# Performance work log

Measured on AMD Instinct MI355X. Metric: run time of the kernel, lower is better.

## Reference

```python
import jax, jax.numpy as jnp
import numpy as np

B, S, H = 2, 2048, 2048
NH, NKV = 16, 4
HD = H // NH          # 128
N_REP = NH // NKV     # 4


def _rotate_half(x):
    x1, x2 = x[..., : x.shape[-1] // 2], x[..., x.shape[-1] // 2 :]
    return jnp.concatenate((-x2, x1), axis=-1)


def setup_inputs() -> dict:
    key = jax.random.key(0)
    ks = jax.random.split(key, 5)
    hidden_states = jax.random.normal(ks[0], (B, S, H), dtype=jnp.float32)
    # true rotary tables [max_seq_len, head_dim]
    inv_freq = 1.0 / (10000.0 ** (np.arange(0, HD, 2, dtype=np.float32) / HD))
    t = np.arange(S, dtype=np.float32)
    freqs = np.outer(t, inv_freq)                    # [S, HD/2]
    emb = np.concatenate([freqs, freqs], axis=-1)    # [S, HD]
    cos = jnp.asarray(np.cos(emb))
    sin = jnp.asarray(np.sin(emb))
    Wq = jax.random.normal(ks[1], (H, NH * HD), dtype=jnp.float32) * 0.02
    Wk = jax.random.normal(ks[2], (H, NKV * HD), dtype=jnp.float32) * 0.02
    Wv = jax.random.normal(ks[3], (H, NKV * HD), dtype=jnp.float32) * 0.02
    Wo = jax.random.normal(ks[4], (NH * HD, H), dtype=jnp.float32) * 0.02
    attention_mask = jnp.ones((B, S), dtype=jnp.float32)  # 1 = keep
    return {"hidden_states": hidden_states, "cos": cos, "sin": sin,
            "Wq": Wq, "Wk": Wk, "Wv": Wv, "Wo": Wo,
            "attention_mask": attention_mask}


def reference(hidden_states, cos, sin, Wq, Wk, Wv, Wo, attention_mask):
    # Decoder self-attention: is_causal=True, use_rope=True, no cache, eval (dropout off).
    x = hidden_states
    b, s, _ = x.shape
    q = jnp.einsum('bsh,hd->bsd', x, Wq).reshape(b, s, NH, HD).transpose(0, 2, 1, 3)   # [b,nh,s,hd]
    k = jnp.einsum('bsh,hd->bsd', x, Wk).reshape(b, s, NKV, HD)
    v = jnp.einsum('bsh,hd->bsd', x, Wv).reshape(b, s, NKV, HD)
    # GQA repeat_kv: each kv head repeated n_rep times contiguously
    k = jnp.repeat(k, N_REP, axis=2).transpose(0, 2, 1, 3)   # [b,nh,s,hd]
    v = jnp.repeat(v, N_REP, axis=2).transpose(0, 2, 1, 3)
    # RoPE
    c = cos[:s][None, None, :, :]
    sn = sin[:s][None, None, :, :]
    q = q * c + _rotate_half(q) * sn
    k = k * c + _rotate_half(k) * sn
    # attention scores
    scores = jnp.einsum('bhqd,bhkd->bhqk', q, k) / jnp.sqrt(jnp.float32(HD))
    neg_inf = jnp.finfo(scores.dtype).min
    causal = jnp.triu(jnp.full((s, s), neg_inf, dtype=scores.dtype), k=1)
    scores = scores + causal[None, None, :, :]
    pad = (1.0 - attention_mask[:, None, None, :].astype(scores.dtype)) * neg_inf
    scores = scores + pad
    attn = jax.nn.softmax(scores.astype(jnp.float32), axis=-1).astype(q.dtype)
    out = jnp.einsum('bhqk,bhkd->bhqd', attn, v)             # [b,nh,s,hd]
    out = out.transpose(0, 2, 1, 3).reshape(b, s, NH * HD)
    return jnp.einsum('bsd,dh->bsh', out, Wo)
```

## Files before the change

### kernel.cpp

```cpp
#include <hip/hip_runtime.h>
#include <hip/hip_bf16.h>


typedef __bf16 bf16;
typedef __bf16 bf16x8 __attribute__((ext_vector_type(8)));
typedef __bf16 bf16x4 __attribute__((ext_vector_type(4)));
typedef float  f32x4  __attribute__((ext_vector_type(4)));

#define MFMA_BF16(a, b, c) __builtin_amdgcn_mfma_f32_16x16x32_bf16((a), (b), (c), 0, 0, 0)

__device__ __forceinline__ void glds16(const bf16* g, char* l) {
  __builtin_amdgcn_global_load_lds((__attribute__((address_space(1))) const void*)g,
                                   (__attribute__((address_space(3))) void*)l, 16, 0, 0);
}

__global__ __launch_bounds__(256) void k_cvt_bf16(const float* __restrict__ in,
                                                  bf16* __restrict__ out, int n4) {
  int i = blockIdx.x * 256 + threadIdx.x;
  if (i < n4) {
    float4 v = ((const float4*)in)[i];
    bf16x4 o;
    o[0] = (bf16)v.x; o[1] = (bf16)v.y; o[2] = (bf16)v.z; o[3] = (bf16)v.w;
    ((bf16x4*)out)[i] = o;
  }
}

__global__ __launch_bounds__(256) void k_transpose_w4(const float* __restrict__ Wq,
                                                      const float* __restrict__ Wk,
                                                      const float* __restrict__ Wv,
                                                      const float* __restrict__ Wo,
                                                      bf16* __restrict__ Wtq,
                                                      bf16* __restrict__ Wtk,
                                                      bf16* __restrict__ Wtv,
                                                      bf16* __restrict__ Wto) {
  int z = blockIdx.z;
  const float* W; bf16* Wt; int N;
  if (z == 0)      { W = Wq; Wt = Wtq; N = 2048; }
  else if (z == 1) { W = Wo; Wt = Wto; N = 2048; }
  else if (z == 2) { W = Wk; Wt = Wtk; N = 512; }
  else             { W = Wv; Wt = Wtv; N = 512; }
  int nb = blockIdx.y * 32;
  if (nb >= N) return;
  __shared__ float tile[32][33];
  int tx = threadIdx.x, ty = threadIdx.y;
  int kb = blockIdx.x * 32;
#pragma unroll
  for (int i = 0; i < 4; ++i)
    tile[ty + i * 8][tx] = W[(size_t)(kb + ty + i * 8) * N + nb + tx];
  __syncthreads();
#pragma unroll
  for (int i = 0; i < 4; ++i)
    Wt[(size_t)(nb + ty + i * 8) * 2048 + kb + tx] = (bf16)tile[tx][ty + i * 8];
}

template <typename OUT>
__device__ void gemm_block(const bf16* __restrict__ A, const bf16* __restrict__ Bt,
                           OUT* __restrict__ C, int K, int ldc,
                           int rbase, int cbase, char* sm,
                           float rope_scl, const float* __restrict__ cosb,
                           const float* __restrict__ sinb,
                           bf16* __restrict__ vtr, int vkv) {
  const int tid = threadIdx.x;
  const int lane = tid & 63, wid = tid >> 6;
  const int l15 = lane & 15, lg = lane >> 4;
  char* Asm = sm;
  char* Bsm = sm + 32768;

  f32x4 acc[2][8];
#pragma unroll
  for (int i = 0; i < 2; ++i)
#pragma unroll
    for (int j = 0; j < 8; ++j)
#pragma unroll
      for (int r = 0; r < 4; ++r) acc[i][j][r] = 0.0f;

  const int ob = wid * 4096 + lane * 16;
  auto stage = [&](int buf, int kb) {
#pragma unroll
    for (int c = 0; c < 4; ++c) {
      int o = ob + c * 1024;
      int r = o >> 7;
      int cc = ((o >> 4) & 7) ^ (r & 7);
      int dst = wid * 4096 + c * 1024 + buf * 16384;
      glds16(A + (size_t)(rbase + r) * K + kb + cc * 8, Asm + dst);
      glds16(Bt + (size_t)(cbase + r) * K + kb + cc * 8, Bsm + dst);
    }
  };

  stage(0, 0);
  __syncthreads();
  const int nk = K >> 6;
  for (int t = 0; t < nk; ++t) {
    if (t + 1 < nk) stage((t + 1) & 1, (t + 1) << 6);
    const char* At  = Asm + (t & 1) * 16384;
    const char* Bti = Bsm + (t & 1) * 16384;
#pragma unroll
    for (int ks = 0; ks < 2; ++ks) {
      bf16x8 a[2], b[8];
#pragma unroll
      for (int rf = 0; rf < 2; ++rf) {
        int r = wid * 32 + rf * 16 + l15;
        int slot = (ks * 4 + lg) ^ (r & 7);
        a[rf] = *(const bf16x8*)(At + r * 128 + slot * 16);
      }
#pragma unroll
      for (int nf = 0; nf < 8; ++nf) {
        int n = nf * 16 + l15;
        int slot = (ks * 4 + lg) ^ (n & 7);
        b[nf] = *(const bf16x8*)(Bti + n * 128 + slot * 16);
      }
#pragma unroll
      for (int rf = 0; rf < 2; ++rf)
#pragma unroll
        for (int nf = 0; nf < 8; ++nf)
          acc[rf][nf] = MFMA_BF16(a[rf], b[nf], acc[rf][nf]);
    }
    __syncthreads();
  }

  if (rope_scl != 0.0f) {
#pragma unroll
    for (int rf = 0; rf < 2; ++rf)
#pragma unroll
      for (int r = 0; r < 4; ++r) {
        int s = (rbase + wid * 32 + rf * 16 + lg * 4 + r) & 2047;
#pragma unroll
        for (int nf = 0; nf < 4; ++nf) {
          int d = nf * 16 + l15;
          float v0 = acc[rf][nf][r], v1 = acc[rf][nf + 4][r];
          float c0 = cosb[s * 128 + d],      c1 = cosb[s * 128 + d + 64];
          float s0 = sinb[s * 128 + d],      s1 = sinb[s * 128 + d + 64];
          acc[rf][nf][r]     = (v0 * c0 - v1 * s0) * rope_scl;
          acc[rf][nf + 4][r] = (v1 * c1 + v0 * s1) * rope_scl;
        }
      }
  }

  if (vtr != nullptr) {
#pragma unroll
    for (int rf = 0; rf < 2; ++rf)
#pragma unroll
      for (int nf = 0; nf < 8; ++nf) {
        int s0 = wid * 32 + rf * 16 + lg * 4;
        int d = nf * 16 + l15;
        bf16x4 pk;
#pragma unroll
        for (int r = 0; r < 4; ++r) pk[r] = (bf16)acc[rf][nf][r];
        *(bf16x4*)(sm + d * 256 + ((s0 * 2) ^ ((d & 15) << 4))) = pk;
      }
    __syncthreads();
    const int b4 = (rbase >> 11) * 4;
    const int scol = rbase & 2047;
    const int so = tid & 15;
#pragma unroll
    for (int i = 0; i < 8; ++i) {
      int d = (tid >> 4) + i * 16;
      bf16x8 v = *(const bf16x8*)(sm + d * 256 + ((so * 16) ^ ((d & 15) << 4)));
      *(bf16x8*)(vtr + (size_t)((b4 + vkv) * 128 + d) * 2048 + scol + so * 8) = v;
    }
    return;
  }

#pragma unroll
  for (int rf = 0; rf < 2; ++rf)
#pragma unroll
    for (int nf = 0; nf < 8; ++nf)
#pragma unroll
      for (int r = 0; r < 4; ++r) {
        int row = rbase + wid * 32 + rf * 16 + lg * 4 + r;
        int col = cbase + nf * 16 + l15;
        C[(size_t)row * ldc + col] = (OUT)acc[rf][nf][r];
      }
}

__global__ __launch_bounds__(256, 2) void k_gemm_qkv(const bf16* __restrict__ X,
                                                     const bf16* __restrict__ Wtq,
                                                     const bf16* __restrict__ Wtk,
                                                     const bf16* __restrict__ Wtv,
                                                     bf16* __restrict__ Q,
                                                     bf16* __restrict__ Ko,
                                                     bf16* __restrict__ Vt,
                                                     const float* __restrict__ cosb,
                                                     const float* __restrict__ sinb,
                                                     float sclq) {
  __shared__ alignas(16) char sm[65536];
  int nb = blockIdx.y;
  int rbase = blockIdx.x * 128;
  if (nb < 16) {
    gemm_block<bf16>(X, Wtq, Q, 2048, 2048, rbase, nb * 128, sm, sclq, cosb, sinb,
                     nullptr, 0);
  } else if (nb < 20) {
    gemm_block<bf16>(X, Wtk, Ko, 2048, 512, rbase, (nb - 16) * 128, sm, 1.0f, cosb, sinb,
                     nullptr, 0);
  } else {
    gemm_block<bf16>(X, Wtv, (bf16*)nullptr, 2048, 512, rbase, (nb - 20) * 128, sm,
                     0.0f, nullptr, nullptr, Vt, nb - 20);
  }
}

__global__ __launch_bounds__(256, 2) void k_gemm_o(const bf16* __restrict__ AO,
                                                   const bf16* __restrict__ Wto,
                                                   float* __restrict__ Out) {
  __shared__ alignas(16) char sm[65536];
  gemm_block<float>(AO, Wto, Out, 2048, 2048, blockIdx.x * 128, blockIdx.y * 128, sm,
                    0.0f, nullptr, nullptr, nullptr, 0);
}

__global__ __launch_bounds__(256, 4) void k_fattn(const bf16* __restrict__ Qg,
                                                  const bf16* __restrict__ Kg,
                                                  const bf16* __restrict__ Vtg,
                                                  bf16* __restrict__ AO) {
  __shared__ alignas(16) char sm[37888];
  const int lane = threadIdx.x & 63, wid = threadIdx.x >> 6;
  const int l15 = lane & 15, lg = lane >> 4;
  const int wg = blockIdx.x;
  const int grp = wg & 7;
  const int b = grp >> 2, kv = grp & 3;
  const int inner = wg >> 3;
  const int h = kv * 4 + (inner & 3);
  const int strip = 31 - (inner >> 2);
  const int q0 = strip * 64 + wid * 16;
  const int nt = 2 * (strip + 1);
  char* Pw = sm + 32768 + wid * 1280;

  bf16x8 qf[4];
#pragma unroll
  for (int kf = 0; kf < 4; ++kf)
    qf[kf] = *(const bf16x8*)(Qg + (size_t)(b * 2048 + q0 + l15) * 2048 + h * 128 + kf * 32 + lg * 8);

  f32x4 o[8];
#pragma unroll
  for (int j = 0; j < 8; ++j)
#pragma unroll
    for (int r = 0; r < 4; ++r) o[j][r] = 0.0f;
  float mrun = -3e38f, lrun = 0.0f;

  const bf16* ksrc[2];
  const bf16* vsrc[2];
  int kdst[2], vdst[2];
#pragma unroll
  for (int j = 0; j < 2; ++j) {
    int c = wid * 128 + j * 64 + lane;
    int kr = c >> 4, kslot = c & 15;
    int kcc = kslot ^ (kr & 15);
    ksrc[j] = Kg + (size_t)(b * 2048 + kr) * 512 + kv * 128 + kcc * 8;
    kdst[j] = wid * 2048 + j * 1024;
    int vr = c >> 2, vslot = c & 3;
    int vcc = vslot ^ ((vr >> 1) & 3);
    vsrc[j] = Vtg + (size_t)((b * 4 + kv) * 128 + vr) * 2048 + vcc * 8;
    vdst[j] = 16384 + wid * 2048 + j * 1024;
  }
  auto stageKV = [&](int buf) {
#pragma unroll
    for (int j = 0; j < 2; ++j) {
      glds16(ksrc[j], sm + buf * 8192 + kdst[j]);
      glds16(vsrc[j], sm + buf * 8192 + vdst[j]);
      ksrc[j] += 32 * 512;
      vsrc[j] += 32;
    }
  };

  stageKV(0);
  __syncthreads();

  for (int t = 0; t < nt; ++t) {
    const int kb = t << 5;
    if (t + 1 < nt) stageKV((t + 1) & 1);
    const char* Kt = sm + (t & 1) * 8192;
    const char* Vt = sm + 16384 + (t & 1) * 8192;

    f32x4 sa[2];
#pragma unroll
    for (int j = 0; j < 2; ++j)
#pragma unroll
      for (int r = 0; r < 4; ++r) sa[j][r] = 0.0f;
    __builtin_amdgcn_s_setprio(1);
#pragma unroll
    for (int kf = 0; kf < 4; ++kf) {
#pragma unroll
      for (int nf = 0; nf < 2; ++nf) {
        int slot = (kf * 4 + lg) ^ l15;
        bf16x8 bk = *(const bf16x8*)(Kt + (nf * 16 + l15) * 256 + slot * 16);
        sa[nf] = MFMA_BF16(bk, qf[kf], sa[nf]);
      }
    }
    __builtin_amdgcn_s_setprio(0);

    if (kb + 31 > q0) {
      const int qi = q0 + l15;
#pragma unroll
      for (int nf = 0; nf < 2; ++nf)
#pragma unroll
        for (int r = 0; r < 4; ++r)
          if (kb + nf * 16 + lg * 4 + r > qi) sa[nf][r] = -3e38f;
    }

    float mx = sa[0][0];
#pragma unroll
    for (int nf = 0; nf < 2; ++nf)
#pragma unroll
      for (int r = 0; r < 4; ++r) mx = fmaxf(mx, sa[nf][r]);
    mx = fmaxf(mx, __shfl_xor(mx, 16));
    mx = fmaxf(mx, __shfl_xor(mx, 32));
    if (!__all(mx - mrun <= 8.0f)) {
      float mnew = fmaxf(mrun, mx);
      float fac = __builtin_amdgcn_exp2f(mrun - mnew);
      lrun *= fac;
      f32x4 fv;
#pragma unroll
      for (int r = 0; r < 4; ++r) fv[r] = __shfl(fac, lg * 4 + r);
#pragma unroll
      for (int j = 0; j < 8; ++j) o[j] *= fv;
      mrun = mnew;
    }
    float rs = 0.0f;
#pragma unroll
    for (int nf = 0; nf < 2; ++nf) {
      bf16x4 pk;
#pragma unroll
      for (int r = 0; r < 4; ++r) {
        float p = __builtin_amdgcn_exp2f(sa[nf][r] - mrun);
        rs += p;
        pk[r] = (bf16)p;
      }
      *(bf16x4*)(Pw + l15 * 80 + nf * 32 + lg * 8) = pk;
    }
    rs += __shfl_xor(rs, 16);
    rs += __shfl_xor(rs, 32);
    lrun += rs;

    bf16x8 pa = *(const bf16x8*)(Pw + l15 * 80 + lg * 16);
    __builtin_amdgcn_s_setprio(1);
#pragma unroll
    for (int nf2 = 0; nf2 < 8; ++nf2) {
      int d = nf2 * 16 + l15;
      int slot = lg ^ ((d >> 1) & 3);
      bf16x8 vb = *(const bf16x8*)(Vt + d * 64 + slot * 16);
      o[nf2] = MFMA_BF16(pa, vb, o[nf2]);
    }
    __builtin_amdgcn_s_setprio(0);
    __syncthreads();
  }

  f32x4 linv;
#pragma unroll
  for (int r = 0; r < 4; ++r) linv[r] = 1.0f / __shfl(lrun, lg * 4 + r);
#pragma unroll
  for (int j = 0; j < 8; ++j)
#pragma unroll
    for (int r = 0; r < 4; ++r) {
      size_t row = (size_t)(b * 2048 + q0 + lg * 4 + r);
      AO[row * 2048 + h * 128 + j * 16 + l15] = (bf16)(o[j][r] * linv[r]);
    }
}

extern "C" void kernel_launch(void* const* d_in, const int* in_sizes, int n_in,
                              void* d_out, int out_size, void* d_ws, size_t ws_size,
                              hipStream_t stream) {
  const float* hs   = (const float*)d_in[0];
  const float* cosb = (const float*)d_in[1];
  const float* sinb = (const float*)d_in[2];
  const float* Wq   = (const float*)d_in[3];
  const float* Wk   = (const float*)d_in[4];
  const float* Wv   = (const float*)d_in[5];
  const float* Wo   = (const float*)d_in[6];
  float* Out = (float*)d_out;

  char* ws = (char*)d_ws;
  size_t off = 0;
  auto alloc = [&](size_t bytes) { char* p = ws + off; off += bytes; return p; };
  bf16* Xbf = (bf16*)alloc((size_t)4096 * 2048 * 2);
  bf16* Wtq = (bf16*)alloc((size_t)2048 * 2048 * 2);
  bf16* Wtk = (bf16*)alloc((size_t)512 * 2048 * 2);
  bf16* Wtv = (bf16*)alloc((size_t)512 * 2048 * 2);
  bf16* Wto = (bf16*)alloc((size_t)2048 * 2048 * 2);
  bf16* Qb  = (bf16*)alloc((size_t)4096 * 2048 * 2);
  bf16* Kb  = (bf16*)alloc((size_t)4096 * 512 * 2);
  bf16* Vtb = (bf16*)alloc((size_t)4096 * 512 * 2);
  bf16* AO  = (bf16*)alloc((size_t)4096 * 2048 * 2);

  const float SCLQ = 0.08838834764831845f * 1.4426950408889634f;

  dim3 tb(32, 8);
  k_cvt_bf16<<<8192, 256, 0, stream>>>(hs, Xbf, 2097152);
  k_transpose_w4<<<dim3(64, 64, 4), tb, 0, stream>>>(Wq, Wk, Wv, Wo, Wtq, Wtk, Wtv, Wto);
  k_gemm_qkv<<<dim3(32, 24), 256, 0, stream>>>(Xbf, Wtq, Wtk, Wtv, Qb, Kb, Vtb,
                                               cosb, sinb, SCLQ);
  k_fattn<<<1024, 256, 0, stream>>>(Qb, Kb, Vtb, AO);
  k_gemm_o<<<dim3(32, 16), 256, 0, stream>>>(AO, Wto, Out);
}
```

Baseline: 202.1 us.

## Pair long and short causal strips per attention block with triple-buffered KV

The flash-attention kernel now gives each block two query strips, one long (31-pair) and one short (pair), so every block does the same total causal work, and launches half as many blocks. KV staging moves from double to triple buffering with an explicit vmcnt wait plus barrier instead of __syncthreads, which keeps two tiles in flight. The cost is more LDS per block and a lower occupancy hint (2 instead of 4 blocks), which reduces latency hiding across waves.

```diff
diff --git a/kernel.cpp b/kernel.cpp
--- a/kernel.cpp
+++ b/kernel.cpp
@@ -206,11 +206,11 @@
                     0.0f, nullptr, nullptr, nullptr, 0);
 }
 
-__global__ __launch_bounds__(256, 4) void k_fattn(const bf16* __restrict__ Qg,
+__global__ __launch_bounds__(256, 2) void k_fattn(const bf16* __restrict__ Qg,
                                                   const bf16* __restrict__ Kg,
                                                   const bf16* __restrict__ Vtg,
                                                   bf16* __restrict__ AO) {
-  __shared__ alignas(16) char sm[37888];
+  __shared__ alignas(16) char sm[54272];
   const int lane = threadIdx.x & 63, wid = threadIdx.x >> 6;
   const int l15 = lane & 15, lg = lane >> 4;
   const int wg = blockIdx.x;
@@ -218,15 +218,19 @@
   const int b = grp >> 2, kv = grp & 3;
   const int inner = wg >> 3;
   const int h = kv * 4 + (inner & 3);
-  const int strip = 31 - (inner >> 2);
-  const int q0 = strip * 64 + wid * 16;
-  const int nt = 2 * (strip + 1);
-  char* Pw = sm + 32768 + wid * 1280;
-
-  bf16x8 qf[4];
-#pragma unroll
-  for (int kf = 0; kf < 4; ++kf)
-    qf[kf] = *(const bf16x8*)(Qg + (size_t)(b * 2048 + q0 + l15) * 2048 + h * 128 + kf * 32 + lg * 8);
+  const int pair = inner >> 2;
+  const int sA = 31 - pair, sB = pair;
+  const int nA = 2 * (sA + 1);
+  const int NT = nA + 2 * (sB + 1);
+  const int q0A = sA * 64 + wid * 16, q0B = sB * 64 + wid * 16;
+  char* Pw = sm + 49152 + wid * 1280;
+
+  bf16x8 qfA[4], qfB[4];
+#pragma unroll
+  for (int kf = 0; kf < 4; ++kf) {
+    qfA[kf] = *(const bf16x8*)(Qg + (size_t)(b * 2048 + q0A + l15) * 2048 + h * 128 + kf * 32 + lg * 8);
+    qfB[kf] = *(const bf16x8*)(Qg + (size_t)(b * 2048 + q0B + l15) * 2048 + h * 128 + kf * 32 + lg * 8);
+  }
 
   f32x4 o[8];
 #pragma unroll
@@ -235,39 +239,37 @@
     for (int r = 0; r < 4; ++r) o[j][r] = 0.0f;
   float mrun = -3e38f, lrun = 0.0f;
 
-  const bf16* ksrc[2];
-  const bf16* vsrc[2];
+  const bf16* ksrc0[2];
+  const bf16* vsrc0[2];
   int kdst[2], vdst[2];
 #pragma unroll
   for (int j = 0; j < 2; ++j) {
     int c = wid * 128 + j * 64 + lane;
     int kr = c >> 4, kslot = c & 15;
     int kcc = kslot ^ (kr & 15);
-    ksrc[j] = Kg + (size_t)(b * 2048 + kr) * 512 + kv * 128 + kcc * 8;
+    ksrc0[j] = Kg + (size_t)(b * 2048 + kr) * 512 + kv * 128 + kcc * 8;
     kdst[j] = wid * 2048 + j * 1024;
     int vr = c >> 2, vslot = c & 3;
     int vcc = vslot ^ ((vr >> 1) & 3);
-    vsrc[j] = Vtg + (size_t)((b * 4 + kv) * 128 + vr) * 2048 + vcc * 8;
-    vdst[j] = 16384 + wid * 2048 + j * 1024;
-  }
-  auto stageKV = [&](int buf) {
+    vsrc0[j] = Vtg + (size_t)((b * 4 + kv) * 128 + vr) * 2048 + vcc * 8;
+    vdst[j] = 8192 + wid * 2048 + j * 1024;
+  }
+
+  auto stage = [&](int i) {
+    if (i >= NT) return;
+    int kb = ((i < nA) ? i : i - nA) << 5;
+    char* bb = sm + (i % 3) * 16384;
 #pragma unroll
     for (int j = 0; j < 2; ++j) {
-      glds16(ksrc[j], sm + buf * 8192 + kdst[j]);
-      glds16(vsrc[j], sm + buf * 8192 + vdst[j]);
-      ksrc[j] += 32 * 512;
-      vsrc[j] += 32;
+      glds16(ksrc0[j] + (size_t)kb * 512, bb + kdst[j]);
+      glds16(vsrc0[j] + kb, bb + vdst[j]);
     }
   };
 
-  stageKV(0);
-  __syncthreads();
-
-  for (int t = 0; t < nt; ++t) {
-    const int kb = t << 5;
-    if (t + 1 < nt) stageKV((t + 1) & 1);
-    const char* Kt = sm + (t & 1) * 8192;
-    const char* Vt = sm + 16384 + (t & 1) * 8192;
+  auto tile = [&](int t, int kb, const bf16x8 (&qf)[4], int q0) {
+    stage(t + 2);
+    const char* Kt = sm + (t % 3) * 16384;
+    const char* Vt = Kt + 8192;
 
     f32x4 sa[2];
 #pragma unroll
@@ -339,19 +341,43 @@
       o[nf2] = MFMA_BF16(pa, vb, o[nf2]);
     }
     __builtin_amdgcn_s_setprio(0);
-    __syncthreads();
-  }
-
-  f32x4 linv;
-#pragma unroll
-  for (int r = 0; r < 4; ++r) linv[r] = 1.0f / __shfl(lrun, lg * 4 + r);
+
+    if (t + 2 < NT) {
+      asm volatile("s_waitcnt vmcnt(4)" ::: "memory");
+      __builtin_amdgcn_s_barrier();
+    } else if (t + 1 < NT) {
+      asm volatile("s_waitcnt vmcnt(0)" ::: "memory");
+      __builtin_amdgcn_s_barrier();
+    }
+  };
+
+  auto epi = [&](int q0) {
+    f32x4 linv;
+#pragma unroll
+    for (int r = 0; r < 4; ++r) linv[r] = 1.0f / __shfl(lrun, lg * 4 + r);
+#pragma unroll
+    for (int j = 0; j < 8; ++j)
+#pragma unroll
+      for (int r = 0; r < 4; ++r) {
+        size_t row = (size_t)(b * 2048 + q0 + lg * 4 + r);
+        AO[row * 2048 + h * 128 + j * 16 + l15] = (bf16)(o[j][r] * linv[r]);
+      }
+  };
+
+  stage(0);
+  stage(1);
+  asm volatile("s_waitcnt vmcnt(4)" ::: "memory");
+  __builtin_amdgcn_s_barrier();
+
+  for (int t = 0; t < nA; ++t) tile(t, t << 5, qfA, q0A);
+  epi(q0A);
 #pragma unroll
   for (int j = 0; j < 8; ++j)
 #pragma unroll
-    for (int r = 0; r < 4; ++r) {
-      size_t row = (size_t)(b * 2048 + q0 + lg * 4 + r);
-      AO[row * 2048 + h * 128 + j * 16 + l15] = (bf16)(o[j][r] * linv[r]);
-    }
+    for (int r = 0; r < 4; ++r) o[j][r] = 0.0f;
+  mrun = -3e38f; lrun = 0.0f;
+  for (int t = nA; t < NT; ++t) tile(t, (t - nA) << 5, qfB, q0B);
+  epi(q0B);
 }
 
 extern "C" void kernel_launch(void* const* d_in, const int* in_sizes, int n_in,
@@ -386,6 +412,6 @@
   k_transpose_w4<<<dim3(64, 64, 4), tb, 0, stream>>>(Wq, Wk, Wv, Wo, Wtq, Wtk, Wtv, Wto);
   k_gemm_qkv<<<dim3(32, 24), 256, 0, stream>>>(Xbf, Wtq, Wtk, Wtv, Qb, Kb, Vtb,
                                                cosb, sinb, SCLQ);
-  k_fattn<<<1024, 256, 0, stream>>>(Qb, Kb, Vtb, AO);
+  k_fattn<<<512, 256, 0, stream>>>(Qb, Kb, Vtb, AO);
   k_gemm_o<<<dim3(32, 16), 256, 0, stream>>>(AO, Wto, Out);
 }
```

New measurement: 203.6 us. About the same (+0.8%).

## Pair causal strips per block, widen KV tiles to 64, keep P in registers

Applied to the files above, without the earlier changes.

Each flash-attention workgroup now handles two query strips, a long one and a short one, so work is balanced across the 512 blocks. KV tiles grow from 32 to 64 keys with 64KB of double-buffered LDS. P is passed to the PV MFMA through lane shuffles and packed bf16 conversion instead of a round trip through LDS. Occupancy drops from 4 to 2 blocks per CU and the grid halves, which may reduce latency hiding.

```diff
diff --git a/kernel.cpp b/kernel.cpp
--- a/kernel.cpp
+++ b/kernel.cpp
@@ -206,11 +206,11 @@
                     0.0f, nullptr, nullptr, nullptr, 0);
 }
 
-__global__ __launch_bounds__(256, 4) void k_fattn(const bf16* __restrict__ Qg,
+__global__ __launch_bounds__(256, 2) void k_fattn(const bf16* __restrict__ Qg,
                                                   const bf16* __restrict__ Kg,
                                                   const bf16* __restrict__ Vtg,
                                                   bf16* __restrict__ AO) {
-  __shared__ alignas(16) char sm[37888];
+  __shared__ alignas(16) char sm[65536];
   const int lane = threadIdx.x & 63, wid = threadIdx.x >> 6;
   const int l15 = lane & 15, lg = lane >> 4;
   const int wg = blockIdx.x;
@@ -218,78 +218,76 @@
   const int b = grp >> 2, kv = grp & 3;
   const int inner = wg >> 3;
   const int h = kv * 4 + (inner & 3);
-  const int strip = 31 - (inner >> 2);
-  const int q0 = strip * 64 + wid * 16;
-  const int nt = 2 * (strip + 1);
-  char* Pw = sm + 32768 + wid * 1280;
+  const int pair = inner >> 2;
+  const int sA = 31 - pair, sB = pair;
+  const int nA = sA + 1;
+  const int NT = nA + sB + 1;
+  const int q0A = sA * 64 + wid * 16, q0B = sB * 64 + wid * 16;
+
+  const bf16 *ks[4], *vs[4];
+#pragma unroll
+  for (int i = 0; i < 4; ++i) {
+    int c = wid * 256 + i * 64 + lane;
+    int kr = c >> 4, kcc = (c & 15) ^ (kr & 15);
+    ks[i] = Kg + (size_t)(b * 2048 + kr) * 512 + kv * 128 + kcc * 8;
+    int vr = c >> 3, vcc = (c & 7) ^ (vr & 7);
+    vs[i] = Vtg + (size_t)((b * 4 + kv) * 128 + vr) * 2048 + vcc * 8;
+  }
+
+  auto stage = [&](int t) {
+    if (t >= NT) return;
+    int kb = ((t < nA) ? t : t - nA) << 6;
+    char* base = sm + (t & 1) * 32768 + wid * 4096;
+#pragma unroll
+    for (int i = 0; i < 4; ++i) {
+      glds16(ks[i] + (size_t)kb * 512, base + i * 1024);
+      glds16(vs[i] + kb, base + 16384 + i * 1024);
+    }
+  };
 
   bf16x8 qf[4];
-#pragma unroll
-  for (int kf = 0; kf < 4; ++kf)
-    qf[kf] = *(const bf16x8*)(Qg + (size_t)(b * 2048 + q0 + l15) * 2048 + h * 128 + kf * 32 + lg * 8);
-
   f32x4 o[8];
-#pragma unroll
-  for (int j = 0; j < 8; ++j)
-#pragma unroll
-    for (int r = 0; r < 4; ++r) o[j][r] = 0.0f;
-  float mrun = -3e38f, lrun = 0.0f;
-
-  const bf16* ksrc[2];
-  const bf16* vsrc[2];
-  int kdst[2], vdst[2];
-#pragma unroll
-  for (int j = 0; j < 2; ++j) {
-    int c = wid * 128 + j * 64 + lane;
-    int kr = c >> 4, kslot = c & 15;
-    int kcc = kslot ^ (kr & 15);
-    ksrc[j] = Kg + (size_t)(b * 2048 + kr) * 512 + kv * 128 + kcc * 8;
-    kdst[j] = wid * 2048 + j * 1024;
-    int vr = c >> 2, vslot = c & 3;
-    int vcc = vslot ^ ((vr >> 1) & 3);
-    vsrc[j] = Vtg + (size_t)((b * 4 + kv) * 128 + vr) * 2048 + vcc * 8;
-    vdst[j] = 16384 + wid * 2048 + j * 1024;
-  }
-  auto stageKV = [&](int buf) {
-#pragma unroll
-    for (int j = 0; j < 2; ++j) {
-      glds16(ksrc[j], sm + buf * 8192 + kdst[j]);
-      glds16(vsrc[j], sm + buf * 8192 + vdst[j]);
-      ksrc[j] += 32 * 512;
-      vsrc[j] += 32;
-    }
-  };
-
-  stageKV(0);
-  __syncthreads();
-
-  for (int t = 0; t < nt; ++t) {
-    const int kb = t << 5;
-    if (t + 1 < nt) stageKV((t + 1) & 1);
-    const char* Kt = sm + (t & 1) * 8192;
-    const char* Vt = sm + 16384 + (t & 1) * 8192;
-
-    f32x4 sa[2];
-#pragma unroll
-    for (int j = 0; j < 2; ++j)
+  float mrun, lrun;
+
+  auto loadQ = [&](int q0) {
+#pragma unroll
+    for (int kf = 0; kf < 4; ++kf)
+      qf[kf] = *(const bf16x8*)(Qg + (size_t)(b * 2048 + q0 + l15) * 2048 + h * 128 + kf * 32 + lg * 8);
+  };
+  auto resetS = [&]() {
+#pragma unroll
+    for (int j = 0; j < 8; ++j)
+#pragma unroll
+      for (int r = 0; r < 4; ++r) o[j][r] = 0.0f;
+    mrun = -3e38f; lrun = 0.0f;
+  };
+
+  auto tile = [&](int t, int kb, int q0, bool diag) {
+    stage(t + 1);
+    const char* Kt = sm + (t & 1) * 32768;
+    const char* Vt = Kt + 16384;
+
+    f32x4 sa[4];
+#pragma unroll
+    for (int j = 0; j < 4; ++j)
 #pragma unroll
       for (int r = 0; r < 4; ++r) sa[j][r] = 0.0f;
     __builtin_amdgcn_s_setprio(1);
 #pragma unroll
     for (int kf = 0; kf < 4; ++kf) {
-#pragma unroll
-      for (int nf = 0; nf < 2; ++nf) {
-        int slot = (kf * 4 + lg) ^ l15;
+      int slot = (kf * 4 + lg) ^ l15;
+#pragma unroll
+      for (int nf = 0; nf < 4; ++nf) {
         bf16x8 bk = *(const bf16x8*)(Kt + (nf * 16 + l15) * 256 + slot * 16);
         sa[nf] = MFMA_BF16(bk, qf[kf], sa[nf]);
       }
     }
     __builtin_amdgcn_s_setprio(0);
 
-    if (kb + 31 > q0) {
+    if (diag) {
       const int qi = q0 + l15;
 #pragma unroll
-      for (int nf = 0; nf < 2; ++nf)
+      for (int nf = 0; nf < 4; ++nf)
 #pragma unroll
         for (int r = 0; r < 4; ++r)
           if (kb + nf * 16 + lg * 4 + r > qi) sa[nf][r] = -3e38f;
@@ -297,7 +295,7 @@
 
     float mx = sa[0][0];
 #pragma unroll
-    for (int nf = 0; nf < 2; ++nf)
+    for (int nf = 0; nf < 4; ++nf)
 #pragma unroll
       for (int r = 0; r < 4; ++r) mx = fmaxf(mx, sa[nf][r]);
     mx = fmaxf(mx, __shfl_xor(mx, 16));
@@ -314,44 +312,79 @@
       mrun = mnew;
     }
     float rs = 0.0f;
-#pragma unroll
-    for (int nf = 0; nf < 2; ++nf) {
-      bf16x4 pk;
-#pragma unroll
-      for (int r = 0; r < 4; ++r) {
-        float p = __builtin_amdgcn_exp2f(sa[nf][r] - mrun);
-        rs += p;
-        pk[r] = (bf16)p;
-      }
-      *(bf16x4*)(Pw + l15 * 80 + nf * 32 + lg * 8) = pk;
+    uint32_t u0[4], u1[4];
+#pragma unroll
+    for (int nf = 0; nf < 4; ++nf) {
+      float p0 = __builtin_amdgcn_exp2f(sa[nf][0] - mrun);
+      float p1 = __builtin_amdgcn_exp2f(sa[nf][1] - mrun);
+      float p2 = __builtin_amdgcn_exp2f(sa[nf][2] - mrun);
+      float p3 = __builtin_amdgcn_exp2f(sa[nf][3] - mrun);
+      rs += (p0 + p1) + (p2 + p3);
+      asm("v_cvt_pk_bf16_f32 %0, %1, %2" : "=v"(u0[nf]) : "v"(p0), "v"(p1));
+      asm("v_cvt_pk_bf16_f32 %0, %1, %2" : "=v"(u1[nf]) : "v"(p2), "v"(p3));
     }
     rs += __shfl_xor(rs, 16);
     rs += __shfl_xor(rs, 32);
     lrun += rs;
 
-    bf16x8 pa = *(const bf16x8*)(Pw + l15 * 80 + lg * 16);
+    uint32_t quad[4][4];
+#pragma unroll
+    for (int nf = 0; nf < 4; ++nf) {
+      uint32_t x0 = (uint32_t)__shfl_xor((int)u0[nf], 16);
+      uint32_t x1 = (uint32_t)__shfl_xor((int)u1[nf], 16);
+      bool ev = (lg & 1) == 0;
+      quad[nf][0] = ev ? u0[nf] : x0;
+      quad[nf][1] = ev ? u1[nf] : x1;
+      quad[nf][2] = ev ? x0 : u0[nf];
+      quad[nf][3] = ev ? x1 : u1[nf];
+    }
+    union UV { uint32_t u[4]; bf16x8 v; } pa0, pa1;
+#pragma unroll
+    for (int i = 0; i < 4; ++i) {
+      uint32_t s0 = (lg & 1) ? quad[0][i] : quad[1][i];
+      uint32_t r0 = (uint32_t)__shfl_xor((int)s0, 32);
+      pa0.u[i] = (lg == 0) ? quad[0][i] : (lg == 3) ? quad[1][i] : r0;
+      uint32_t s1 = (lg & 1) ? quad[2][i] : quad[3][i];
+      uint32_t r1 = (uint32_t)__shfl_xor((int)s1, 32);
+      pa1.u[i] = (lg == 0) ? quad[2][i] : (lg == 3) ? quad[3][i] : r1;
+    }
+
     __builtin_amdgcn_s_setprio(1);
 #pragma unroll
     for (int nf2 = 0; nf2 < 8; ++nf2) {
       int d = nf2 * 16 + l15;
-      int slot = lg ^ ((d >> 1) & 3);
-      bf16x8 vb = *(const bf16x8*)(Vt + d * 64 + slot * 16);
-      o[nf2] = MFMA_BF16(pa, vb, o[nf2]);
+      bf16x8 vb0 = *(const bf16x8*)(Vt + d * 128 + ((lg ^ (d & 7)) * 16));
+      o[nf2] = MFMA_BF16(pa0.v, vb0, o[nf2]);
+      bf16x8 vb1 = *(const bf16x8*)(Vt + d * 128 + (((4 + lg) ^ (d & 7)) * 16));
+      o[nf2] = MFMA_BF16(pa1.v, vb1, o[nf2]);
     }
     __builtin_amdgcn_s_setprio(0);
     __syncthreads();
-  }
-
-  f32x4 linv;
-#pragma unroll
-  for (int r = 0; r < 4; ++r) linv[r] = 1.0f / __shfl(lrun, lg * 4 + r);
-#pragma unroll
-  for (int j = 0; j < 8; ++j)
-#pragma unroll
-    for (int r = 0; r < 4; ++r) {
-      size_t row = (size_t)(b * 2048 + q0 + lg * 4 + r);
-      AO[row * 2048 + h * 128 + j * 16 + l15] = (bf16)(o[j][r] * linv[r]);
-    }
+  };
+
+  auto epi = [&](int q0) {
+    f32x4 linv;
+#pragma unroll
+    for (int r = 0; r < 4; ++r) linv[r] = 1.0f / __shfl(lrun, lg * 4 + r);
+#pragma unroll
+    for (int j = 0; j < 8; ++j)
+#pragma unroll
+      for (int r = 0; r < 4; ++r) {
+        size_t row = (size_t)(b * 2048 + q0 + lg * 4 + r);
+        AO[row * 2048 + h * 128 + j * 16 + l15] = (bf16)(o[j][r] * linv[r]);
+      }
+  };
+
+  stage(0);
+  __syncthreads();
+
+  loadQ(q0A); resetS();
+  for (int t = 0; t < nA; ++t) tile(t, t << 6, q0A, t == nA - 1);
+  epi(q0A);
+
+  loadQ(q0B); resetS();
+  for (int t = nA; t < NT; ++t) tile(t, (t - nA) << 6, q0B, t == NT - 1);
+  epi(q0B);
 }
 
 extern "C" void kernel_launch(void* const* d_in, const int* in_sizes, int n_in,
@@ -386,6 +419,6 @@
   k_transpose_w4<<<dim3(64, 64, 4), tb, 0, stream>>>(Wq, Wk, Wv, Wo, Wtq, Wtk, Wtv, Wto);
   k_gemm_qkv<<<dim3(32, 24), 256, 0, stream>>>(Xbf, Wtq, Wtk, Wtv, Qb, Kb, Vtb,
                                                cosb, sinb, SCLQ);
-  k_fattn<<<1024, 256, 0, stream>>>(Qb, Kb, Vtb, AO);
+  k_fattn<<<512, 256, 0, stream>>>(Qb, Kb, Vtb, AO);
   k_gemm_o<<<dim3(32, 16), 256, 0, stream>>>(AO, Wto, Out);
 }
```

New measurement: 212.6 us. 1.05x slower.
